# Kernel tuning notes

Measured on AMD Instinct MI355X. Metric: run time of the kernel, lower is better.

Reference implementation:

```python
import jax, jax.numpy as jnp
import numpy as np

D = 128        # feature dim (hard-coded 128 split in source)
C = 16         # number of classes
N_S = 1600     # support set size (C * 100 shots)
Q = 32768      # number of query samples
HID = 128      # Class_Adap hidden width


def _class_centers(support_feat_inv, support_features, support_labels):
    # per-class mean of both support tensors (ComputeClassCenters)
    ones = jnp.ones((support_labels.shape[0],), support_feat_inv.dtype)
    counts = jax.ops.segment_sum(ones, support_labels, num_segments=C)
    counts = jnp.maximum(counts, 1.0)[:, None]                     # [C,1]
    mean_s = jax.ops.segment_sum(support_feat_inv, support_labels, num_segments=C) / counts   # [C,D]
    pre_s = jax.ops.segment_sum(support_features, support_labels, num_segments=C) / counts    # [C,D]
    return mean_s, pre_s


def setup_inputs() -> dict:
    key = jax.random.key(0)
    ks = jax.random.split(key, 6)
    return {
        "support_feat_inv": jax.random.normal(ks[0], (N_S, D), jnp.float32),
        "support_features": jax.random.normal(ks[1], (N_S, D), jnp.float32),
        "query_features": jax.random.normal(ks[2], (Q, D), jnp.float32),
        "W1": jax.random.normal(ks[3], (2 * D + 1, HID), jnp.float32) * 0.05,
        "b1": jnp.zeros((HID,), jnp.float32),
        "W2": jax.random.normal(ks[4], (HID, 1), jnp.float32) * 0.05,
        "b2": jnp.zeros((1,), jnp.float32),
        "support_labels": jax.random.randint(ks[5], (N_S,), 0, C),
        "query_labels": jax.random.randint(jax.random.fold_in(key, 7), (Q,), 0, C),
    }


def reference(support_feat_inv, support_features, query_features, W1, b1, W2, b2,
              support_labels, query_labels) -> jnp.ndarray:
    mean_s, pre_s = _class_centers(support_feat_inv, support_features, support_labels)
    q = query_features[:, None, :]                                  # [Q,1,D]
    gated = jax.nn.sigmoid(mean_s)[None, :, :] * q                  # [Q,C,D]
    q_full = jnp.broadcast_to(q, gated.shape)                       # [Q,C,D]
    inp = jnp.concatenate([q_full, gated], axis=-1)                 # [Q,C,2D]
    # AdaptiveAvgPool2d((None, D)) on [C,1,2D]: average adjacent pairs along last dim
    pooled = inp.reshape(Q, C, D, 2).mean(axis=-1)                  # [Q,C,D]
    # inner/outer product: sum(pre_support * query) per class
    outer = jnp.sum(pre_s[None, :, :] * q, axis=-1, keepdims=True)  # [Q,C,1]
    ext = jnp.concatenate([inp, outer], axis=-1)                    # [Q,C,2D+1]
    # Class_Adap tiny MLP -> per-class scalar weight
    h = jax.nn.relu(jnp.einsum('qce,eh->qch', ext, W1) + b1)        # [Q,C,HID]
    w = jax.nn.sigmoid(jnp.einsum('qch,ho->qco', h, W2) + b2)       # [Q,C,1]
    agg = jnp.sum(pooled * w, axis=1)                               # [Q,D]
    return agg + query_features                                     # residual (query_feature[0])
```

## Files before the change

kernel.cpp:

```cpp
#include <hip/hip_runtime.h>
#include <hip/hip_bf16.h>
#include <stdint.h>

#define DD 128
#define CC 16
#define NS 1600
#define QQ 32768
#define NBLK 64

typedef __attribute__((ext_vector_type(8))) short short8;
typedef __attribute__((ext_vector_type(4))) short short4v;
typedef __attribute__((ext_vector_type(4))) float f32x4;

__device__ inline short f2bf(float x) {
  union { float f; uint32_t u; } v; v.f = x;
  uint32_t r = (v.u + 0x7FFFu + ((v.u >> 16) & 1u)) >> 16;
  return (short)r;
}

__device__ inline uint32_t pk2bf(float lo, float hi) {
  __hip_bfloat162 h = __float22bfloat162_rn(make_float2(lo, hi));
  union { __hip_bfloat162 h2; uint32_t u; } v; v.h2 = h;
  return v.u;
}

__global__ __launch_bounds__(256) void prep_kernel(
    const float* __restrict__ sfi, const float* __restrict__ sf,
    const int* __restrict__ labels, const float* __restrict__ qf,
    float* __restrict__ partA, float* __restrict__ partB,
    float* __restrict__ pcnt, short* __restrict__ qbf) {
  const int t = threadIdx.x;

  if (blockIdx.x >= NBLK) {
    const size_t cb = (size_t)(blockIdx.x - NBLK) * (128 * DD);
#pragma unroll
    for (int i = 0; i < 16; ++i) {
      const size_t off = cb + ((size_t)i * 256 + t) * 4;
      f32x4 f = *(const f32x4*)(qf + off);
      union { short4v s; uint32_t u[2]; } r;
      r.u[0] = pk2bf(f[0], f[1]);
      r.u[1] = pk2bf(f[2], f[3]);
      *(short4v*)(qbf + off) = r.s;
    }
    return;
  }

  __shared__ float accA[2][CC][DD];
  __shared__ float accB[2][CC][DD];
  __shared__ float cnt[2][CC];
  const int d = t & 127, s = t >> 7;
  for (int i = t; i < 2 * CC * DD; i += 256) {
    ((float*)accA)[i] = 0.f;
    ((float*)accB)[i] = 0.f;
  }
  if (t < 2 * CC) ((float*)cnt)[t] = 0.f;
  __syncthreads();

  const int base = blockIdx.x * (NS / NBLK);
  for (int i = s; i < NS / NBLK; i += 2) {
    const int r = base + i;
    const int lbl = labels[r];
    accA[s][lbl][d] += sfi[(size_t)r * DD + d];
    accB[s][lbl][d] += sf[(size_t)r * DD + d];
    if (d == 0) cnt[s][lbl] += 1.f;
  }
  __syncthreads();

  float* pa = partA + (size_t)blockIdx.x * (CC * DD);
  float* pb = partB + (size_t)blockIdx.x * (CC * DD);
  for (int i = t; i < CC * DD; i += 256) {
    pa[i] = ((float*)accA)[i] + ((float*)accA)[CC * DD + i];
    pb[i] = ((float*)accB)[i] + ((float*)accB)[CC * DD + i];
  }
  if (t < CC) pcnt[blockIdx.x * CC + t] = cnt[0][t] + cnt[1][t];
}

__global__ __launch_bounds__(256) void build_wt_kernel(
    const float* __restrict__ W1, const float* __restrict__ partA,
    const float* __restrict__ partB, const float* __restrict__ pcnt,
    float* __restrict__ sg_out, short* __restrict__ WtTg) {
  __shared__ float sgc[DD], prc[DD];
  const int c = blockIdx.x, t = threadIdx.x;

  float cnt = 0.f;
  for (int b = 0; b < NBLK; ++b) cnt += pcnt[b * CC + c];
  cnt = fmaxf(cnt, 1.f);
  if (t < 128) {
    float a = 0.f;
    for (int b = 0; b < NBLK; ++b) a += partA[(size_t)b * (CC * DD) + c * DD + t];
    const float m = a / cnt;
    const float s = 1.f / (1.f + expf(-m));
    sgc[t] = s;
    sg_out[c * DD + t] = s;
  } else {
    const int d = t - 128;
    float a = 0.f;
    for (int b = 0; b < NBLK; ++b) a += partB[(size_t)b * (CC * DD) + c * DD + d];
    prc[d] = a / cnt;
  }
  __syncthreads();

  for (int it = 0; it < 8; ++it) {
    const int u = it * 256 + t;
    const int w_ = u >> 8;
    const int kb = (u >> 6) & 3;
    const int lane = u & 63;
    const int j = w_ * 16 + (lane & 15);
    const int e0 = kb * 32 + (lane >> 4) * 8;
    short8 r;
#pragma unroll
    for (int rr = 0; rr < 8; ++rr) {
      const int e = e0 + rr;
      float v = W1[e * DD + j] + sgc[e] * W1[(DD + e) * DD + j] +
                prc[e] * W1[2 * DD * DD + j];
      r[rr] = f2bf(v);
    }
    *(short8*)(WtTg + ((size_t)c * 2048 + u) * 8) = r;
  }
}

__global__ __launch_bounds__(512, 4) void main_kernel(
    const short* __restrict__ qbf, const short* __restrict__ WtTg,
    const float* __restrict__ b1, const float* __restrict__ W2,
    const float* __restrict__ b2, float* __restrict__ w_ws) {
  __shared__ float p_part[8][CC][64];

  const int tid = threadIdx.x;
  const int lane = tid & 63;
  const int w = tid >> 6;
  const int l15 = lane & 15, l4 = lane >> 4;
  const int qbase = blockIdx.x * 64;

  short8 bq[4][4];
#pragma unroll
  for (int qn = 0; qn < 4; ++qn) {
    const short* qrow = qbf + (size_t)(qbase + qn * 16 + l15) * DD;
#pragma unroll
    for (int kb = 0; kb < 4; ++kb)
      bq[qn][kb] = *(const short8*)(qrow + kb * 32 + l4 * 8);
  }

  const f32x4 b1v = *(const f32x4*)(b1 + w * 16 + l4 * 4);
  const f32x4 w2v = *(const f32x4*)(W2 + w * 16 + l4 * 4);
  const float b2s = b2[0];

  const char* wbase = (const char*)WtTg + w * 4096 + lane * 16;

#define LOADW(dst, cls)                                                     \
  {                                                                         \
    _Pragma("unroll") for (int kb = 0; kb < 4; ++kb) dst[kb] =              \
        *(const short8*)(wbase + (size_t)(cls)*32768 + kb * 1024);          \
  }

#define COMPUTE(wf, cls)                                                    \
  {                                                                         \
    _Pragma("unroll") for (int qp = 0; qp < 2; ++qp) {                      \
      f32x4 a0 = b1v, a1 = b1v;                                             \
      _Pragma("unroll") for (int kb = 0; kb < 4; ++kb) {                    \
        a0 = __builtin_amdgcn_mfma_f32_16x16x32_bf16(wf[kb],                \
                                                     bq[2 * qp][kb], a0,    \
                                                     0, 0, 0);              \
        a1 = __builtin_amdgcn_mfma_f32_16x16x32_bf16(wf[kb],                \
                                                     bq[2 * qp + 1][kb],    \
                                                     a1, 0, 0, 0);          \
      }                                                                     \
      float p0 = 0.f, p1 = 0.f;                                             \
      _Pragma("unroll") for (int i = 0; i < 4; ++i) {                       \
        p0 += fmaxf(a0[i], 0.f) * w2v[i];                                   \
        p1 += fmaxf(a1[i], 0.f) * w2v[i];                                   \
      }                                                                     \
      p0 += __shfl_xor(p0, 16);                                             \
      p0 += __shfl_xor(p0, 32);                                             \
      p1 += __shfl_xor(p1, 16);                                             \
      p1 += __shfl_xor(p1, 32);                                             \
      if (l4 == 0) {                                                        \
        p_part[w][cls][(2 * qp) * 16 + l15] = p0;                           \
        p_part[w][cls][(2 * qp + 1) * 16 + l15] = p1;                       \
      }                                                                     \
    }                                                                       \
  }

  short8 wfA[4], wfB[4];
  LOADW(wfA, 0);
  for (int c = 0; c < CC; c += 2) {
    LOADW(wfB, c + 1);
    COMPUTE(wfA, c);
    if (c + 2 < CC) LOADW(wfA, c + 2);
    COMPUTE(wfB, c + 1);
  }
#undef LOADW
#undef COMPUTE

  __syncthreads();

  {
    const int q = tid & 63;
    const int cg = tid >> 6;
    float s0 = 0.f, s1 = 0.f;
#pragma unroll
    for (int wv = 0; wv < 8; ++wv) {
      s0 += p_part[wv][cg * 2][q];
      s1 += p_part[wv][cg * 2 + 1][q];
    }
    float2 o;
    o.x = 1.f / (1.f + __expf(-(s0 + b2s)));
    o.y = 1.f / (1.f + __expf(-(s1 + b2s)));
    *(float2*)(w_ws + ((size_t)(qbase + q)) * 16 + cg * 2) = o;
  }
}

__global__ __launch_bounds__(256) void agg_kernel(
    const float* __restrict__ qf, const float* __restrict__ sg,
    const float* __restrict__ w_ws, float* __restrict__ out) {
  const int t = threadIdx.x;
  const int s = t >> 5;
  const int ec = t & 31;
  const int e0 = ec * 4;
  const int qbase = blockIdx.x * 64;

  float4 sgv[16];
#pragma unroll
  for (int c = 0; c < 16; ++c) sgv[c] = *(const float4*)(sg + c * DD + e0);

  for (int qi = 0; qi < 8; ++qi) {
    const int q = qbase + qi * 8 + s;
    const float* wr = w_ws + (size_t)q * 16;
    float4 w0 = *(const float4*)(wr);
    float4 w1 = *(const float4*)(wr + 4);
    float4 w2 = *(const float4*)(wr + 8);
    float4 w3 = *(const float4*)(wr + 12);
    const float wc[16] = {w0.x, w0.y, w0.z, w0.w, w1.x, w1.y, w1.z, w1.w,
                          w2.x, w2.y, w2.z, w2.w, w3.x, w3.y, w3.z, w3.w};
    float Sv = 0.f;
#pragma unroll
    for (int c = 0; c < 16; ++c) Sv += wc[c];

    f32x4 sgw = {0.f, 0.f, 0.f, 0.f};
#pragma unroll
    for (int c = 0; c < 16; ++c) {
      sgw.x += wc[c] * sgv[c].x;
      sgw.y += wc[c] * sgv[c].y;
      sgw.z += wc[c] * sgv[c].z;
      sgw.w += wc[c] * sgv[c].w;
    }

    const float* qrow = qf + (size_t)q * DD;
    float4 qa = *(const float4*)(qrow + e0);
    float2 qd = *(const float2*)(qrow + 2 * ec);
    float2 qu = *(const float2*)(qrow + 64 + 2 * ec);

    float2 lo, hi;
    lo.x = 0.5f * (qa.x + qa.y) * Sv + qd.x;
    lo.y = 0.5f * (qa.z + qa.w) * Sv + qd.y;
    hi.x = 0.5f * (qa.x * sgw.x + qa.y * sgw.y) + qu.x;
    hi.y = 0.5f * (qa.z * sgw.z + qa.w * sgw.w) + qu.y;

    float* orow = out + (size_t)q * DD;
    *(float2*)(orow + 2 * ec) = lo;
    *(float2*)(orow + 64 + 2 * ec) = hi;
  }
}

extern "C" void kernel_launch(void* const* d_in, const int* in_sizes, int n_in,
                              void* d_out, int out_size, void* d_ws, size_t ws_size,
                              hipStream_t stream) {
  const float* sfi = (const float*)d_in[0];
  const float* sf  = (const float*)d_in[1];
  const float* qf  = (const float*)d_in[2];
  const float* W1  = (const float*)d_in[3];
  const float* b1  = (const float*)d_in[4];
  const float* W2  = (const float*)d_in[5];
  const float* b2  = (const float*)d_in[6];
  const int* slab  = (const int*)d_in[7];
  float* out = (float*)d_out;

  float* sg    = (float*)d_ws;
  float* w_ws  = sg + CC * DD;
  short* WtTg  = (short*)(w_ws + (size_t)QQ * CC);
  float* partA = (float*)(WtTg + CC * DD * DD);
  float* partB = partA + NBLK * CC * DD;
  float* pcnt  = partB + NBLK * CC * DD;
  short* qbf   = (short*)(pcnt + NBLK * CC);

  prep_kernel<<<NBLK + QQ / 128, 256, 0, stream>>>(sfi, sf, slab, qf, partA,
                                                   partB, pcnt, qbf);
  build_wt_kernel<<<CC, 256, 0, stream>>>(W1, partA, partB, pcnt, sg, WtTg);
  main_kernel<<<QQ / 64, 512, 0, stream>>>(qbf, WtTg, b1, W2, b2, w_ws);
  agg_kernel<<<QQ / 64, 256, 0, stream>>>(qf, sg, w_ws, out);
}
```

Before: 57.22 us.

## Split main kernel by class, stage class weights in swizzled LDS via direct loads

```diff
diff --git a/kernel.cpp b/kernel.cpp
--- a/kernel.cpp
+++ b/kernel.cpp
@@ -101,12 +101,10 @@
   __syncthreads();
 
   for (int it = 0; it < 8; ++it) {
-    const int u = it * 256 + t;
-    const int w_ = u >> 8;
-    const int kb = (u >> 6) & 3;
-    const int lane = u & 63;
-    const int j = w_ * 16 + (lane & 15);
-    const int e0 = kb * 32 + (lane >> 4) * 8;
+    const int p = it * 256 + t;
+    const int j = it * 16 + (t >> 4);
+    const int eb = (t & 15) ^ ((t >> 4) & 7);
+    const int e0 = eb * 8;
     short8 r;
 #pragma unroll
     for (int rr = 0; rr < 8; ++rr) {
@@ -115,21 +113,31 @@
                 prc[e] * W1[2 * DD * DD + j];
       r[rr] = f2bf(v);
     }
-    *(short8*)(WtTg + ((size_t)c * 2048 + u) * 8) = r;
-  }
-}
-
-__global__ __launch_bounds__(512, 4) void main_kernel(
+    *(short8*)(WtTg + ((size_t)c * 2048 + p) * 8) = r;
+  }
+}
+
+__global__ __launch_bounds__(256, 4) void main_kernel(
     const short* __restrict__ qbf, const short* __restrict__ WtTg,
     const float* __restrict__ b1, const float* __restrict__ W2,
     const float* __restrict__ b2, float* __restrict__ w_ws) {
-  __shared__ float p_part[8][CC][64];
+  __shared__ __align__(16) char Wl[32768];
 
   const int tid = threadIdx.x;
   const int lane = tid & 63;
   const int w = tid >> 6;
   const int l15 = lane & 15, l4 = lane >> 4;
-  const int qbase = blockIdx.x * 64;
+  const int cls = blockIdx.x & 15;
+  const int qbase = (blockIdx.x >> 4) * 256 + w * 64;
+
+  const char* gsrc = (const char*)WtTg + (size_t)cls * 32768;
+#pragma unroll
+  for (int i = 0; i < 8; ++i) {
+    const int off = i * 4096 + tid * 16;
+    __builtin_amdgcn_global_load_lds(
+        (const __attribute__((address_space(1))) uint32_t*)(gsrc + off),
+        (__attribute__((address_space(3))) uint32_t*)(&Wl[0] + off), 16, 0, 0);
+  }
 
   short8 bq[4][4];
 #pragma unroll
@@ -139,73 +147,48 @@
     for (int kb = 0; kb < 4; ++kb)
       bq[qn][kb] = *(const short8*)(qrow + kb * 32 + l4 * 8);
   }
-
-  const f32x4 b1v = *(const f32x4*)(b1 + w * 16 + l4 * 4);
-  const f32x4 w2v = *(const f32x4*)(W2 + w * 16 + l4 * 4);
   const float b2s = b2[0];
 
-  const char* wbase = (const char*)WtTg + w * 4096 + lane * 16;
-
-#define LOADW(dst, cls)                                                     \
-  {                                                                         \
-    _Pragma("unroll") for (int kb = 0; kb < 4; ++kb) dst[kb] =              \
-        *(const short8*)(wbase + (size_t)(cls)*32768 + kb * 1024);          \
-  }
-
-#define COMPUTE(wf, cls)                                                    \
-  {                                                                         \
-    _Pragma("unroll") for (int qp = 0; qp < 2; ++qp) {                      \
-      f32x4 a0 = b1v, a1 = b1v;                                             \
-      _Pragma("unroll") for (int kb = 0; kb < 4; ++kb) {                    \
-        a0 = __builtin_amdgcn_mfma_f32_16x16x32_bf16(wf[kb],                \
-                                                     bq[2 * qp][kb], a0,    \
-                                                     0, 0, 0);              \
-        a1 = __builtin_amdgcn_mfma_f32_16x16x32_bf16(wf[kb],                \
-                                                     bq[2 * qp + 1][kb],    \
-                                                     a1, 0, 0, 0);          \
-      }                                                                     \
-      float p0 = 0.f, p1 = 0.f;                                             \
-      _Pragma("unroll") for (int i = 0; i < 4; ++i) {                       \
-        p0 += fmaxf(a0[i], 0.f) * w2v[i];                                   \
-        p1 += fmaxf(a1[i], 0.f) * w2v[i];                                   \
-      }                                                                     \
-      p0 += __shfl_xor(p0, 16);                                             \
-      p0 += __shfl_xor(p0, 32);                                             \
-      p1 += __shfl_xor(p1, 16);                                             \
-      p1 += __shfl_xor(p1, 32);                                             \
-      if (l4 == 0) {                                                        \
-        p_part[w][cls][(2 * qp) * 16 + l15] = p0;                           \
-        p_part[w][cls][(2 * qp + 1) * 16 + l15] = p1;                       \
-      }                                                                     \
-    }                                                                       \
-  }
-
-  short8 wfA[4], wfB[4];
-  LOADW(wfA, 0);
-  for (int c = 0; c < CC; c += 2) {
-    LOADW(wfB, c + 1);
-    COMPUTE(wfA, c);
-    if (c + 2 < CC) LOADW(wfA, c + 2);
-    COMPUTE(wfB, c + 1);
-  }
-#undef LOADW
-#undef COMPUTE
-
-  __syncthreads();
-
-  {
-    const int q = tid & 63;
-    const int cg = tid >> 6;
-    float s0 = 0.f, s1 = 0.f;
-#pragma unroll
-    for (int wv = 0; wv < 8; ++wv) {
-      s0 += p_part[wv][cg * 2][q];
-      s1 += p_part[wv][cg * 2 + 1][q];
-    }
-    float2 o;
-    o.x = 1.f / (1.f + __expf(-(s0 + b2s)));
-    o.y = 1.f / (1.f + __expf(-(s1 + b2s)));
-    *(float2*)(w_ws + ((size_t)(qbase + q)) * 16 + cg * 2) = o;
+  asm volatile("s_waitcnt vmcnt(0)" ::: "memory");
+  __syncthreads();
+
+  float pacc[4] = {0.f, 0.f, 0.f, 0.f};
+
+#pragma unroll
+  for (int jm = 0; jm < 8; ++jm) {
+    short8 A[4];
+#pragma unroll
+    for (int kb = 0; kb < 4; ++kb) {
+      const int unit = (jm * 16 + l15) * 16 + ((kb * 4 + l4) ^ (l15 & 7));
+      A[kb] = *(const short8*)(Wl + unit * 16);
+    }
+    const f32x4 b1v = *(const f32x4*)(b1 + jm * 16 + l4 * 4);
+    const f32x4 w2v = *(const f32x4*)(W2 + jm * 16 + l4 * 4);
+
+    f32x4 acc[4];
+#pragma unroll
+    for (int qn = 0; qn < 4; ++qn) acc[qn] = f32x4{0.f, 0.f, 0.f, 0.f};
+#pragma unroll
+    for (int kb = 0; kb < 4; ++kb)
+#pragma unroll
+      for (int qn = 0; qn < 4; ++qn)
+        acc[qn] = __builtin_amdgcn_mfma_f32_16x16x32_bf16(A[kb], bq[qn][kb],
+                                                          acc[qn], 0, 0, 0);
+#pragma unroll
+    for (int qn = 0; qn < 4; ++qn)
+#pragma unroll
+      for (int i = 0; i < 4; ++i)
+        pacc[qn] += fmaxf(acc[qn][i] + b1v[i], 0.f) * w2v[i];
+  }
+
+#pragma unroll
+  for (int qn = 0; qn < 4; ++qn) {
+    float p = pacc[qn];
+    p += __shfl_xor(p, 16);
+    p += __shfl_xor(p, 32);
+    if (l4 == 0)
+      w_ws[(size_t)cls * QQ + qbase + qn * 16 + l15] =
+          1.f / (1.f + __expf(-(p + b2s)));
   }
 }
 
@@ -218,42 +201,33 @@
   const int e0 = ec * 4;
   const int qbase = blockIdx.x * 64;
 
-  float4 sgv[16];
-#pragma unroll
-  for (int c = 0; c < 16; ++c) sgv[c] = *(const float4*)(sg + c * DD + e0);
+  f32x4 sgv[16];
+#pragma unroll
+  for (int c = 0; c < 16; ++c) sgv[c] = *(const f32x4*)(sg + c * DD + e0);
 
   for (int qi = 0; qi < 8; ++qi) {
     const int q = qbase + qi * 8 + s;
-    const float* wr = w_ws + (size_t)q * 16;
-    float4 w0 = *(const float4*)(wr);
-    float4 w1 = *(const float4*)(wr + 4);
-    float4 w2 = *(const float4*)(wr + 8);
-    float4 w3 = *(const float4*)(wr + 12);
-    const float wc[16] = {w0.x, w0.y, w0.z, w0.w, w1.x, w1.y, w1.z, w1.w,
-                          w2.x, w2.y, w2.z, w2.w, w3.x, w3.y, w3.z, w3.w};
+    float wc[16];
     float Sv = 0.f;
 #pragma unroll
-    for (int c = 0; c < 16; ++c) Sv += wc[c];
-
+    for (int c = 0; c < 16; ++c) {
+      wc[c] = w_ws[(size_t)c * QQ + q];
+      Sv += wc[c];
+    }
     f32x4 sgw = {0.f, 0.f, 0.f, 0.f};
 #pragma unroll
-    for (int c = 0; c < 16; ++c) {
-      sgw.x += wc[c] * sgv[c].x;
-      sgw.y += wc[c] * sgv[c].y;
-      sgw.z += wc[c] * sgv[c].z;
-      sgw.w += wc[c] * sgv[c].w;
-    }
+    for (int c = 0; c < 16; ++c) sgw += wc[c] * sgv[c];
 
     const float* qrow = qf + (size_t)q * DD;
-    float4 qa = *(const float4*)(qrow + e0);
+    f32x4 qa = *(const f32x4*)(qrow + e0);
     float2 qd = *(const float2*)(qrow + 2 * ec);
     float2 qu = *(const float2*)(qrow + 64 + 2 * ec);
 
     float2 lo, hi;
-    lo.x = 0.5f * (qa.x + qa.y) * Sv + qd.x;
-    lo.y = 0.5f * (qa.z + qa.w) * Sv + qd.y;
-    hi.x = 0.5f * (qa.x * sgw.x + qa.y * sgw.y) + qu.x;
-    hi.y = 0.5f * (qa.z * sgw.z + qa.w * sgw.w) + qu.y;
+    lo.x = 0.5f * (qa[0] + qa[1]) * Sv + qd.x;
+    lo.y = 0.5f * (qa[2] + qa[3]) * Sv + qd.y;
+    hi.x = 0.5f * (qa[0] * sgw[0] + qa[1] * sgw[1]) + qu.x;
+    hi.y = 0.5f * (qa[2] * sgw[2] + qa[3] * sgw[3]) + qu.y;
 
     float* orow = out + (size_t)q * DD;
     *(float2*)(orow + 2 * ec) = lo;
@@ -275,16 +249,16 @@
   float* out = (float*)d_out;
 
   float* sg    = (float*)d_ws;
-  float* w_ws  = sg + CC * DD;
-  short* WtTg  = (short*)(w_ws + (size_t)QQ * CC);
+  short* WtTg  = (short*)(sg + CC * DD);
   float* partA = (float*)(WtTg + CC * DD * DD);
   float* partB = partA + NBLK * CC * DD;
   float* pcnt  = partB + NBLK * CC * DD;
   short* qbf   = (short*)(pcnt + NBLK * CC);
+  float* w_ws  = (float*)(qbf + (size_t)QQ * DD);
 
   prep_kernel<<<NBLK + QQ / 128, 256, 0, stream>>>(sfi, sf, slab, qf, partA,
                                                    partB, pcnt, qbf);
   build_wt_kernel<<<CC, 256, 0, stream>>>(W1, partA, partB, pcnt, sg, WtTg);
-  main_kernel<<<QQ / 64, 512, 0, stream>>>(qbf, WtTg, b1, W2, b2, w_ws);
+  main_kernel<<<(QQ / 256) * CC, 256, 0, stream>>>(qbf, WtTg, b1, W2, b2, w_ws);
   agg_kernel<<<QQ / 64, 256, 0, stream>>>(qf, sg, w_ws, out);
 }
```

Result: slower. 207.4 us (+262.4%).
